# Kernel tuning notes

Hardware: AMD Instinct MI355X
Metric: run time of the kernel (lower is better)

Reference implementation:

```python
import jax, jax.numpy as jnp
import numpy as np

NUM_NODES = 50000
NUM_EDGES = 600000
NUM_FEAT = 128
HIDDEN = 512
N_OUT = 128
K = 3
N_GRAPHS = 128


def setup_inputs() -> dict:
    key = jax.random.key(0)
    ks = jax.random.split(key, 12)
    feature = jax.random.normal(ks[0], (NUM_NODES, NUM_FEAT), dtype=jnp.float32)
    edge_index = jax.random.randint(ks[1], (2, NUM_EDGES), 0, NUM_NODES, dtype=jnp.int64)
    protein_batch = jnp.sort(jax.random.randint(ks[2], (NUM_NODES,), 0, N_GRAPHS, dtype=jnp.int64))
    s = 0.05
    # ChebConv weights stored [K, in, out] (x @ W), single shared bias per conv
    W1 = jax.random.normal(ks[3], (K, NUM_FEAT, NUM_FEAT), dtype=jnp.float32) * s
    b1 = jax.random.normal(ks[4], (NUM_FEAT,), dtype=jnp.float32) * s
    W2 = jax.random.normal(ks[5], (K, NUM_FEAT, 2 * NUM_FEAT), dtype=jnp.float32) * s
    b2 = jax.random.normal(ks[6], (2 * NUM_FEAT,), dtype=jnp.float32) * s
    fc1_w = jax.random.normal(ks[7], (3 * NUM_FEAT, HIDDEN), dtype=jnp.float32) * s
    fc1_b = jax.random.normal(ks[8], (HIDDEN,), dtype=jnp.float32) * s
    fc2_w = jax.random.normal(ks[9], (HIDDEN, N_OUT), dtype=jnp.float32) * s
    fc2_b = jax.random.normal(ks[10], (N_OUT,), dtype=jnp.float32) * s
    return {"feature": feature, "edge_index": edge_index, "protein_batch": protein_batch,
            "W1": W1, "b1": b1, "W2": W2, "b2": b2,
            "fc1_w": fc1_w, "fc1_b": fc1_b, "fc2_w": fc2_w, "fc2_b": fc2_b}


def _cheb_conv(x, src, dst, edge_w, W, b):
    # PyG ChebConv with sym normalization, lambda_max=2 => scaled Laplacian
    # L_hat has zero diagonal and off-diag weights -1/sqrt(d_i d_j) (edge_w).
    def prop(h):
        return jax.ops.segment_sum(edge_w[:, None] * h[src], dst, num_segments=NUM_NODES)

    Tx0 = x
    out = Tx0 @ W[0]
    Tx1 = prop(x)
    out = out + Tx1 @ W[1]
    for k in range(2, W.shape[0]):
        Tx2 = 2.0 * prop(Tx1) - Tx0
        out = out + Tx2 @ W[k]
        Tx0, Tx1 = Tx1, Tx2
    return out + b


def reference(feature, edge_index, protein_batch, W1, b1, W2, b2, fc1_w, fc1_b, fc2_w, fc2_b):
    src, dst = edge_index[0], edge_index[1]
    deg = jax.ops.segment_sum(jnp.ones_like(src, dtype=feature.dtype), src, num_segments=NUM_NODES)
    dinv = jnp.where(deg > 0, jax.lax.rsqrt(jnp.maximum(deg, 1.0)), 0.0)
    edge_w = -dinv[src] * dinv[dst]  # (2/lambda_max)*L_sym off-diagonal; diag cancels to 0

    gx = jax.nn.relu(_cheb_conv(feature, src, dst, edge_w, W1, b1))
    gx = jax.nn.relu(_cheb_conv(gx, src, dst, edge_w, W2, b2))
    gx = jnp.concatenate([gx, feature], axis=1)  # [N, 3*F]

    # global_mean_pool
    sums = jax.ops.segment_sum(gx, protein_batch, num_segments=N_GRAPHS)
    cnts = jax.ops.segment_sum(jnp.ones((gx.shape[0],), gx.dtype), protein_batch, num_segments=N_GRAPHS)
    pooled = sums / jnp.maximum(cnts, 1.0)[:, None]

    h = jax.nn.relu(pooled @ fc1_w + fc1_b)  # dropout is identity in eval
    return h @ fc2_w + fc2_b
```

## Files before the change

kernel.cpp:

```cpp
#include <hip/hip_runtime.h>
#include <hip/hip_bf16.h>

#define NNODES 50000
#define NEDGES 600000
#define NB 196
#define NBKT 196
#define SB 192
#define SCH (NEDGES / SB)

typedef short vs8 __attribute__((ext_vector_type(8)));
typedef float floatx4 __attribute__((ext_vector_type(4)));

__device__ __forceinline__ float us2f(unsigned short u) {
    unsigned int x = ((unsigned int)u) << 16;
    float f;
    __builtin_memcpy(&f, &x, 4);
    return f;
}
__device__ __forceinline__ unsigned short f2us(float f) {
    unsigned int x;
    __builtin_memcpy(&x, &f, 4);
    unsigned int r = x + 0x7fffu + ((x >> 16) & 1u);
    return (unsigned short)(r >> 16);
}
__device__ __forceinline__ float ldf(const void* p, int i, int ff) {
    if (ff) return us2f(((const unsigned short*)p)[i]);
    return ((const float*)p)[i];
}
__device__ __forceinline__ int2 ldnt_sw(const int2* p) {
    unsigned long long v =
        __builtin_nontemporal_load(reinterpret_cast<const unsigned long long*>(p));
    int2 r;
    r.x = (int)(unsigned int)(v & 0xffffffffULL);
    r.y = (int)(unsigned int)(v >> 32);
    return r;
}
__device__ __forceinline__ void gload_lds16(const unsigned short* g, unsigned short* l) {
    __builtin_amdgcn_global_load_lds(
        (const __attribute__((address_space(1))) unsigned int*)g,
        (__attribute__((address_space(3))) unsigned int*)l, 16, 0, 0);
}
__device__ __forceinline__ void accum8(float w, uint4 u, float& a0, float& a1,
                                       float& a2, float& a3, float& a4, float& a5,
                                       float& a6, float& a7) {
    a0 += w * us2f((unsigned short)(u.x & 0xffffu));
    a1 += w * us2f((unsigned short)(u.x >> 16));
    a2 += w * us2f((unsigned short)(u.y & 0xffffu));
    a3 += w * us2f((unsigned short)(u.y >> 16));
    a4 += w * us2f((unsigned short)(u.z & 0xffffu));
    a5 += w * us2f((unsigned short)(u.z >> 16));
    a6 += w * us2f((unsigned short)(u.w & 0xffffu));
    a7 += w * us2f((unsigned short)(u.w >> 16));
}

__global__ void k_detect(const int* ei, const unsigned int* fw, int* iflag, int* fflag) {
    int lane = threadIdx.x;
    int odd1 = ei[2 * lane + 1];
    int odd2 = ei[128 + 2 * lane + 1];
    unsigned long long nz = __ballot(odd1 != 0 || odd2 != 0);
    unsigned int e = (fw[lane] >> 7) & 0xffu;
    unsigned long long h = __ballot(e > 100u && e < 160u);
    if (lane == 0) {
        *iflag = (nz == 0ULL) ? 1 : 0;
        *fflag = (__popcll(h) > 40) ? 1 : 0;
    }
}

__global__ void k_featb(const void* src, const int* iflag, const int* fflag,
                        const int* pb, int* b32, float* psum, unsigned short* dst) {
    int i = blockIdx.x * 256 + threadIdx.x;
    if (i < NNODES) {
        int f = *iflag;
        b32[i] = pb[((size_t)i) << f];
    }
    if (i < 128 * 384) psum[i] = 0.f;
    if (i >= NNODES * 128 / 8) return;
    if (*fflag) {
        reinterpret_cast<uint4*>(dst)[i] = reinterpret_cast<const uint4*>(src)[i];
    } else {
        const float4* fs = reinterpret_cast<const float4*>(src);
        float4 a = fs[2 * i], b = fs[2 * i + 1];
        uint4 o;
        o.x = (unsigned int)f2us(a.x) | ((unsigned int)f2us(a.y) << 16);
        o.y = (unsigned int)f2us(a.z) | ((unsigned int)f2us(a.w) << 16);
        o.z = (unsigned int)f2us(b.x) | ((unsigned int)f2us(b.y) << 16);
        o.w = (unsigned int)f2us(b.z) | ((unsigned int)f2us(b.w) << 16);
        reinterpret_cast<uint4*>(dst)[i] = o;
    }
}

__global__ __launch_bounds__(256) void k_deghist(const int* ei, const int* iflag,
                                                 unsigned int* degpart, int* cntT) {
    __shared__ unsigned int h[25000];
    __shared__ int c[NBKT];
    int t = threadIdx.x, blk = blockIdx.x;
    for (int i = t; i < 25000; i += 256) h[i] = 0u;
    if (t < NBKT) c[t] = 0;
    __syncthreads();
    int f = *iflag;
    int e0 = blk * SCH;
    for (int j = t; j < SCH; j += 256) {
        int e = e0 + j;
        int s = ei[((size_t)e) << f];
        int d = ei[((size_t)(NEDGES + e)) << f];
        atomicAdd(&h[s >> 1], (s & 1) ? 65536u : 1u);
        atomicAdd(&c[d >> 8], 1);
    }
    __syncthreads();
    unsigned int* dp = degpart + (size_t)blk * 25000;
    for (int i = t; i < 25000; i += 256) dp[i] = h[i];
    if (t < NBKT) cntT[t * SB + blk] = c[t];
}

__global__ void k_dred(const unsigned int* degpart, float* dinv) {
    int i = blockIdx.x * 256 + threadIdx.x;
    if (i >= 25000) return;
    unsigned int lo = 0, hi = 0;
    for (int b = 0; b < SB; ++b) {
        unsigned int p = degpart[(size_t)b * 25000 + i];
        lo += p & 0xffffu;
        hi += p >> 16;
    }
    dinv[2 * i] = lo ? rsqrtf((float)lo) : 0.f;
    dinv[2 * i + 1] = hi ? rsqrtf((float)hi) : 0.f;
}

__global__ void k_bprefix(int* cntT, int* btot) {
    __shared__ int sh[256];
    int t = threadIdx.x, b = blockIdx.x;
    int v = (t < SB) ? cntT[b * SB + t] : 0;
    sh[t] = v;
    __syncthreads();
    for (int off = 1; off < 256; off <<= 1) {
        int x = (t >= off) ? sh[t - off] : 0;
        __syncthreads();
        sh[t] += x;
        __syncthreads();
    }
    if (t < SB) cntT[b * SB + t] = sh[t] - v;
    if (t == 255) btot[b] = sh[255];
}

__global__ void k_bscan2(const int* btot, int* gbase, const int* batch32,
                         int* pcnt, int* rowptr) {
    __shared__ int sh[256];
    int t = threadIdx.x;
    int v = (t < NBKT) ? btot[t] : 0;
    sh[t] = v;
    __syncthreads();
    for (int off = 1; off < 256; off <<= 1) {
        int x = (t >= off) ? sh[t - off] : 0;
        __syncthreads();
        sh[t] += x;
        __syncthreads();
    }
    if (t < NBKT) gbase[t] = sh[t] - v;
    if (t == 0) {
        gbase[NBKT] = NEDGES;
        rowptr[NNODES] = NEDGES;
    }
    if (t < 128) {
        int g = t;
        int lo = 0, hi = NNODES;
        while (lo < hi) { int mid = (lo + hi) >> 1; if (batch32[mid] < g) lo = mid + 1; else hi = mid; }
        int start = lo;
        hi = NNODES;
        while (lo < hi) { int mid = (lo + hi) >> 1; if (batch32[mid] <= g) lo = mid + 1; else hi = mid; }
        pcnt[g] = lo - start;
    }
}

__global__ void k_scat(const int* ei, const int* iflag, const float* dinv,
                       const int* gbase, const int* cntT, int2* bkt) {
    __shared__ int cur[NBKT];
    int t = threadIdx.x, blk = blockIdx.x;
    if (t < NBKT) cur[t] = gbase[t] + cntT[t * SB + blk];
    __syncthreads();
    int f = *iflag;
    int e0 = blk * SCH;
    for (int j = t; j < SCH; j += 256) {
        int e = e0 + j;
        int s = ei[((size_t)e) << f];
        int d = ei[((size_t)(NEDGES + e)) << f];
        float w = -dinv[s] * dinv[d];
        int slot = atomicAdd(&cur[d >> 8], 1);
        int wb;
        __builtin_memcpy(&wb, &w, 4);
        int2 v;
        v.x = s | ((d & 255) << 16);
        v.y = wb;
        bkt[slot] = v;
    }
}

__global__ void k_csr(const int2* bkt, const int* gbase, int* rowptr, int2* csr_sw) {
    __shared__ int hist[256], scan[256], cur[256];
    int t = threadIdx.x, b = blockIdx.x;
    int beg = gbase[b], end = gbase[b + 1];
    int n = end - beg;
    hist[t] = 0;
    __syncthreads();
    for (int i = t; i < n; i += 256) {
        int bin = (bkt[beg + i].x >> 16) & 255;
        atomicAdd(&hist[bin], 1);
    }
    __syncthreads();
    int h = hist[t];
    scan[t] = h;
    __syncthreads();
    for (int off = 1; off < 256; off <<= 1) {
        int x = (t >= off) ? scan[t - off] : 0;
        __syncthreads();
        scan[t] += x;
        __syncthreads();
    }
    int excl = scan[t] - h;
    int node = b * 256 + t;
    if (node < NNODES) rowptr[node] = beg + excl;
    cur[t] = excl;
    __syncthreads();
    for (int i = t; i < n; i += 256) {
        int2 p = bkt[beg + i];
        int bin = (p.x >> 16) & 255;
        int slot = atomicAdd(&cur[bin], 1);
        int2 v;
        v.x = p.x & 0xffff;
        v.y = p.y;
        csr_sw[beg + slot] = v;
    }
}

__global__ void k_prepall(const void* W1, const void* W2, const void* b1, const void* b2,
                          const void* f1w, const void* f1b, const void* f2w, const void* f2b,
                          const int* fflag, unsigned short* W1t, unsigned short* W2t,
                          float* b1f, float* b2f, float* f1wf, float* f1bf,
                          float* f2wf, float* f2bf) {
    int i = blockIdx.x * 256 + threadIdx.x;
    int ff = *fflag;
    if (i < 49152) {
        int c = i >> 13;
        int rem = i & 8191;
        int cr = rem >> 6;
        int rem2 = rem & 63;
        int g = rem2 >> 3, j = rem2 & 7;
        int k = c * 64 + ((g ^ (cr & 7)) << 3) + j;
        int n = cr;
        float v;
        if (k < 128) v = ldf(W1, k * 128 + n, ff) - ldf(W1, (256 + k) * 128 + n, ff);
        else if (k < 256) v = ldf(W1, k * 128 + n, ff);
        else v = 2.f * ldf(W1, k * 128 + n, ff);
        W1t[i] = f2us(v);
        return;
    }
    i -= 49152;
    if (i < 98304) {
        int ct = i / 49152;
        int rem = i % 49152;
        int c = rem >> 13;
        int rem1 = rem & 8191;
        int cr = rem1 >> 6;
        int rem2 = rem1 & 63;
        int g = rem2 >> 3, j = rem2 & 7;
        int k = c * 64 + ((g ^ (cr & 7)) << 3) + j;
        int n = ct * 128 + cr;
        float v;
        if (k < 128) v = ldf(W2, k * 256 + n, ff) - ldf(W2, (256 + k) * 256 + n, ff);
        else if (k < 256) v = ldf(W2, k * 256 + n, ff);
        else v = 2.f * ldf(W2, k * 256 + n, ff);
        W2t[i] = f2us(v);
        return;
    }
    i -= 98304;
    if (i < 196608) { f1wf[i] = ldf(f1w, i, ff); return; }
    i -= 196608;
    if (i < 65536) { f2wf[i] = ldf(f2w, i, ff); return; }
    i -= 65536;
    if (i < 512) { f1bf[i] = ldf(f1b, i, ff); return; }
    i -= 512;
    if (i < 256) { b2f[i] = ldf(b2, i, ff); return; }
    i -= 256;
    if (i < 128) { b1f[i] = ldf(b1, i, ff); return; }
    i -= 128;
    if (i < 128) f2bf[i] = ldf(f2b, i, ff);
}

__global__ __launch_bounds__(256, 6) void k_prop(const unsigned short* X,
                                                 const int* rowptr, const int2* csr_sw,
                                                 unsigned short* out) {
    int wvid = (blockIdx.x * blockDim.x + threadIdx.x) >> 6;
    int lane = threadIdx.x & 63;
    int q = lane >> 4;
    int ln = lane & 15;
    int node = wvid * 4 + q;
    if (node >= NNODES) return;
    int fo = ln * 8;
    int beg = rowptr[node], end = rowptr[node + 1];
    float a0 = 0.f, a1 = 0.f, a2 = 0.f, a3 = 0.f;
    float a4 = 0.f, a5 = 0.f, a6 = 0.f, a7 = 0.f;
    int j = beg;
    for (; j + 8 <= end; j += 8) {
        int2 e0 = ldnt_sw(csr_sw + j);
        int2 e1 = ldnt_sw(csr_sw + j + 1);
        int2 e2 = ldnt_sw(csr_sw + j + 2);
        int2 e3 = ldnt_sw(csr_sw + j + 3);
        int2 e4 = ldnt_sw(csr_sw + j + 4);
        int2 e5 = ldnt_sw(csr_sw + j + 5);
        int2 e6 = ldnt_sw(csr_sw + j + 6);
        int2 e7 = ldnt_sw(csr_sw + j + 7);
        uint4 u0 = *reinterpret_cast<const uint4*>(X + (size_t)e0.x * 128 + fo);
        uint4 u1 = *reinterpret_cast<const uint4*>(X + (size_t)e1.x * 128 + fo);
        uint4 u2 = *reinterpret_cast<const uint4*>(X + (size_t)e2.x * 128 + fo);
        uint4 u3 = *reinterpret_cast<const uint4*>(X + (size_t)e3.x * 128 + fo);
        uint4 u4 = *reinterpret_cast<const uint4*>(X + (size_t)e4.x * 128 + fo);
        uint4 u5 = *reinterpret_cast<const uint4*>(X + (size_t)e5.x * 128 + fo);
        uint4 u6 = *reinterpret_cast<const uint4*>(X + (size_t)e6.x * 128 + fo);
        uint4 u7 = *reinterpret_cast<const uint4*>(X + (size_t)e7.x * 128 + fo);
        float w0, w1, w2, w3, w4, w5, w6, w7;
        __builtin_memcpy(&w0, &e0.y, 4);
        __builtin_memcpy(&w1, &e1.y, 4);
        __builtin_memcpy(&w2, &e2.y, 4);
        __builtin_memcpy(&w3, &e3.y, 4);
        __builtin_memcpy(&w4, &e4.y, 4);
        __builtin_memcpy(&w5, &e5.y, 4);
        __builtin_memcpy(&w6, &e6.y, 4);
        __builtin_memcpy(&w7, &e7.y, 4);
        accum8(w0, u0, a0, a1, a2, a3, a4, a5, a6, a7);
        accum8(w1, u1, a0, a1, a2, a3, a4, a5, a6, a7);
        accum8(w2, u2, a0, a1, a2, a3, a4, a5, a6, a7);
        accum8(w3, u3, a0, a1, a2, a3, a4, a5, a6, a7);
        accum8(w4, u4, a0, a1, a2, a3, a4, a5, a6, a7);
        accum8(w5, u5, a0, a1, a2, a3, a4, a5, a6, a7);
        accum8(w6, u6, a0, a1, a2, a3, a4, a5, a6, a7);
        accum8(w7, u7, a0, a1, a2, a3, a4, a5, a6, a7);
    }
    for (; j + 4 <= end; j += 4) {
        int2 e0 = ldnt_sw(csr_sw + j);
        int2 e1 = ldnt_sw(csr_sw + j + 1);
        int2 e2 = ldnt_sw(csr_sw + j + 2);
        int2 e3 = ldnt_sw(csr_sw + j + 3);
        uint4 u0 = *reinterpret_cast<const uint4*>(X + (size_t)e0.x * 128 + fo);
        uint4 u1 = *reinterpret_cast<const uint4*>(X + (size_t)e1.x * 128 + fo);
        uint4 u2 = *reinterpret_cast<const uint4*>(X + (size_t)e2.x * 128 + fo);
        uint4 u3 = *reinterpret_cast<const uint4*>(X + (size_t)e3.x * 128 + fo);
        float w0, w1, w2, w3;
        __builtin_memcpy(&w0, &e0.y, 4);
        __builtin_memcpy(&w1, &e1.y, 4);
        __builtin_memcpy(&w2, &e2.y, 4);
        __builtin_memcpy(&w3, &e3.y, 4);
        accum8(w0, u0, a0, a1, a2, a3, a4, a5, a6, a7);
        accum8(w1, u1, a0, a1, a2, a3, a4, a5, a6, a7);
        accum8(w2, u2, a0, a1, a2, a3, a4, a5, a6, a7);
        accum8(w3, u3, a0, a1, a2, a3, a4, a5, a6, a7);
    }
    for (; j < end; ++j) {
        int2 e = ldnt_sw(csr_sw + j);
        float w;
        __builtin_memcpy(&w, &e.y, 4);
        uint4 u = *reinterpret_cast<const uint4*>(X + (size_t)e.x * 128 + fo);
        accum8(w, u, a0, a1, a2, a3, a4, a5, a6, a7);
    }
    uint4 ov;
    ov.x = (unsigned int)f2us(a0) | ((unsigned int)f2us(a1) << 16);
    ov.y = (unsigned int)f2us(a2) | ((unsigned int)f2us(a3) << 16);
    ov.z = (unsigned int)f2us(a4) | ((unsigned int)f2us(a5) << 16);
    ov.w = (unsigned int)f2us(a6) | ((unsigned int)f2us(a7) << 16);
    *reinterpret_cast<uint4*>(out + (size_t)node * 128 + fo) = ov;
}

template <int POOL, int CT>
__global__ __launch_bounds__(512, 4) void k_convg(
    const unsigned short* seg0, const unsigned short* seg1, const unsigned short* seg2,
    const unsigned short* Wt, const float* bias, unsigned short* out,
    const int* batch32, float* psum) {
    __shared__ __align__(16) unsigned short a_lds[2][8192];
    __shared__ __align__(16) unsigned short b_lds[2][8192];
    __shared__ float sh_ps[POOL ? 1024 : 1];
    int tid = threadIdx.x;
    int bid = blockIdx.x;
    int grp = 8 * CT;
    int main_blocks = 48 * grp;
    int r, ct;
    if (bid < main_blocks) {
        int g = bid / grp;
        int rem = bid - g * grp;
        ct = rem >> 3;
        r = g * 8 + (rem & 7);
    } else {
        int t = bid - main_blocks;
        r = 384 + (CT == 1 ? t : t % 7);
        ct = (CT == 1) ? 0 : t / 7;
    }
    int r0 = r * 128;
    const unsigned short* segs[3] = {seg0, seg1, seg2};
    int wv = tid >> 6, lane = tid & 63;
    int wm = wv >> 2, wn = wv & 3;
    int m = lane & 15, kq = lane >> 4;
    if (POOL) { sh_ps[tid] = 0.f; sh_ps[tid + 512] = 0.f; }

    auto STAGE = [&](int buf, int c) {
        const unsigned short* S = segs[c >> 1];
        int h = c & 1;
#pragma unroll
        for (int p = 0; p < 2; ++p) {
            int q = wv * 2 + p;
            int rl = q * 8 + (lane >> 3);
            int g = lane & 7;
            int rowg = r0 + rl;
            if (rowg >= NNODES) rowg = NNODES - 1;
            gload_lds16(S + (size_t)rowg * 128 + h * 64 + ((g ^ (rl & 7)) << 3),
                        &a_lds[buf][q * 512]);
        }
#pragma unroll
        for (int p = 0; p < 2; ++p) {
            int q = wv * 2 + p;
            gload_lds16(Wt + (size_t)(ct * 6 + c) * 8192 + q * 512 + (lane << 3),
                        &b_lds[buf][q * 512]);
        }
    };

    floatx4 acc[4][2];
#pragma unroll
    for (int mt = 0; mt < 4; ++mt)
#pragma unroll
        for (int nt = 0; nt < 2; ++nt) {
            acc[mt][nt][0] = 0.f; acc[mt][nt][1] = 0.f;
            acc[mt][nt][2] = 0.f; acc[mt][nt][3] = 0.f;
        }

    STAGE(0, 0);
    __syncthreads();
    int buf = 0;
#pragma unroll
    for (int c = 0; c < 6; ++c) {
        if (c < 5) STAGE(buf ^ 1, c + 1);
        vs8 af[4], bfr[2];
#pragma unroll
        for (int kf = 0; kf < 2; ++kf) {
            int G = kf * 4 + kq;
#pragma unroll
            for (int mt = 0; mt < 4; ++mt) {
                int row = wm * 64 + mt * 16 + m;
                af[mt] = *reinterpret_cast<const vs8*>(
                    &a_lds[buf][row * 64 + ((G ^ (row & 7)) << 3)]);
            }
#pragma unroll
            for (int nt = 0; nt < 2; ++nt) {
                int cl = wn * 32 + nt * 16 + m;
                bfr[nt] = *reinterpret_cast<const vs8*>(
                    &b_lds[buf][cl * 64 + ((G ^ (cl & 7)) << 3)]);
            }
#pragma unroll
            for (int mt = 0; mt < 4; ++mt)
#pragma unroll
                for (int nt = 0; nt < 2; ++nt)
                    acc[mt][nt] = __builtin_amdgcn_mfma_f32_16x16x32_bf16(
                        af[mt], bfr[nt], acc[mt][nt], 0, 0, 0);
        }
        if (c < 5) {
            __syncthreads();
            buf ^= 1;
        }
    }

    if (POOL == 0) {
#pragma unroll
        for (int mt = 0; mt < 4; ++mt) {
            int rbase = r0 + wm * 64 + mt * 16 + kq * 4;
#pragma unroll
            for (int nt = 0; nt < 2; ++nt) {
                int col = wn * 32 + nt * 16 + m;
                float bv = bias[col];
#pragma unroll
                for (int i = 0; i < 4; ++i) {
                    int rw = rbase + i;
                    if (rw < NNODES) {
                        float v = acc[mt][nt][i] + bv;
                        v = v > 0.f ? v : 0.f;
                        out[(size_t)rw * 128 + col] = f2us(v);
                    }
                }
            }
        }
    } else {
        int g0 = batch32[r0];
#pragma unroll
        for (int mt = 0; mt < 4; ++mt) {
            int rbase = r0 + wm * 64 + mt * 16 + kq * 4;
            int gid[4];
#pragma unroll
            for (int i = 0; i < 4; ++i) {
                int rw = rbase + i;
                gid[i] = rw < NNODES ? batch32[rw] : -1;
            }
#pragma unroll
            for (int nt = 0; nt < 2; ++nt) {
                int cl = wn * 32 + nt * 16 + m;
                int col = ct * 128 + cl;
                float bv = bias[col];
                float run = 0.f;
                int curg = -1;
#pragma unroll
                for (int i = 0; i < 4; ++i) {
                    int g = gid[i];
                    if (g < 0) break;
                    float v = acc[mt][nt][i] + bv;
                    v = v > 0.f ? v : 0.f;
                    if (g != curg) {
                        if (curg >= 0) {
                            int gl = curg - g0;
                            if (gl >= 0 && gl < 8) atomicAdd(&sh_ps[gl * 128 + cl], run);
                            else atomicAdd(&psum[curg * 384 + col], run);
                        }
                        curg = g;
                        run = 0.f;
                    }
                    run += v;
                }
                if (curg >= 0) {
                    int gl = curg - g0;
                    if (gl >= 0 && gl < 8) atomicAdd(&sh_ps[gl * 128 + cl], run);
                    else atomicAdd(&psum[curg * 384 + col], run);
                }
            }
        }
        __syncthreads();
        for (int idx = tid; idx < 1024; idx += 512) {
            int gl = idx >> 7, cl = idx & 127;
            float v = sh_ps[idx];
            int gg = g0 + gl;
            if (v != 0.f && gg < 128) atomicAdd(&psum[(size_t)gg * 384 + ct * 128 + cl], v);
        }
    }
}

__global__ void k_poolnodes(const unsigned short* featb, const int* batch32, float* psum) {
    int col = threadIdx.x & 127;
    int half = threadIdx.x >> 7;
    int nbeg = blockIdx.x * 128 + half * 64;
    if (nbeg >= NNODES) return;
    int nend = nbeg + 64;
    if (nend > NNODES) nend = NNODES;
    float run = 0.f;
    int curg = batch32[nbeg];
    for (int n = nbeg; n < nend; ++n) {
        int g = batch32[n];
        if (g != curg) {
            atomicAdd(&psum[curg * 384 + 256 + col], run);
            run = 0.f;
            curg = g;
        }
        run += us2f(featb[(size_t)n * 128 + col]);
    }
    atomicAdd(&psum[curg * 384 + 256 + col], run);
}

__global__ void k_fc1(const float* psum, const int* pcnt, const float* w,
                      const float* b, float* h) {
    int g = blockIdx.x, j = threadIdx.x * 2;
    int c = pcnt[g];
    float inv = 1.f / (float)(c > 0 ? c : 1);
    float a0 = 0.f, a1 = 0.f;
    for (int k = 0; k < 384; ++k) {
        float p = psum[g * 384 + k];
        a0 += p * w[k * 512 + j];
        a1 += p * w[k * 512 + j + 1];
    }
    a0 = a0 * inv + b[j];
    a1 = a1 * inv + b[j + 1];
    h[g * 512 + j] = a0 > 0.f ? a0 : 0.f;
    h[g * 512 + j + 1] = a1 > 0.f ? a1 : 0.f;
}

__global__ void ChebModel_74380243632480_kernel(const float* h, const float* w,
                                                const float* b, const int* fflag,
                                                void* out) {
    int g = blockIdx.x, j = threadIdx.x;
    float acc = 0.f;
    for (int k = 0; k < 512; ++k) acc += h[g * 512 + k] * w[k * 128 + j];
    acc += b[j];
    if (*fflag) ((unsigned short*)out)[g * 128 + j] = f2us(acc);
    else ((float*)out)[g * 128 + j] = acc;
}

extern "C" void kernel_launch(void* const* d_in, const int* in_sizes, int n_in,
                              void* d_out, int out_size, void* d_ws, size_t ws_size,
                              hipStream_t stream) {
    const void* feature = d_in[0];
    const int* edge_index = (const int*)d_in[1];
    const int* batch = (const int*)d_in[2];
    const void* W1 = d_in[3];
    const void* b1 = d_in[4];
    const void* W2 = d_in[5];
    const void* b2 = d_in[6];
    const void* fc1w = d_in[7];
    const void* fc1b = d_in[8];
    const void* fc2w = d_in[9];
    const void* fc2b = d_in[10];

    char* ws = (char*)d_ws;
    size_t off = 0;
    int* iflag = (int*)(ws + off); off += 256;
    int* fflag = (int*)(ws + off); off += 256;
    int* rowptr = (int*)(ws + off); off += ((size_t)(NNODES + 1) * 4 + 255) & ~(size_t)255;
    float* dinv = (float*)(ws + off); off += ((size_t)NNODES * 4 + 255) & ~(size_t)255;
    int* batch32 = (int*)(ws + off); off += ((size_t)NNODES * 4 + 255) & ~(size_t)255;
    int* gbase = (int*)(ws + off); off += 1024;
    int* cntT = (int*)(ws + off); off += ((size_t)SB * NBKT * 4 + 255) & ~(size_t)255;
    int* btot = (int*)(ws + off); off += 1024;
    int2* csr_sw = (int2*)(ws + off); off += ((size_t)NEDGES * 8 + 255) & ~(size_t)255;
    unsigned short* featb = (unsigned short*)(ws + off); off += ((size_t)NNODES * 128 * 2 + 255) & ~(size_t)255;
    unsigned short* T1 = (unsigned short*)(ws + off); off += ((size_t)NNODES * 128 * 2 + 255) & ~(size_t)255;
    unsigned short* T2 = (unsigned short*)(ws + off); off += ((size_t)NNODES * 128 * 2 + 255) & ~(size_t)255;
    unsigned short* gx1 = (unsigned short*)(ws + off); off += ((size_t)NNODES * 128 * 2 + 255) & ~(size_t)255;
    unsigned short* W1t = (unsigned short*)(ws + off); off += ((size_t)49152 * 2 + 255) & ~(size_t)255;
    unsigned short* W2t = (unsigned short*)(ws + off); off += ((size_t)98304 * 2 + 255) & ~(size_t)255;
    float* b1f = (float*)(ws + off); off += 1024;
    float* b2f = (float*)(ws + off); off += 1024;
    float* fc1wf = (float*)(ws + off); off += ((size_t)196608 * 4 + 255) & ~(size_t)255;
    float* fc1bf = (float*)(ws + off); off += 2048;
    float* fc2wf = (float*)(ws + off); off += ((size_t)65536 * 4 + 255) & ~(size_t)255;
    float* fc2bf = (float*)(ws + off); off += 1024;
    float* psum = (float*)(ws + off); off += ((size_t)128 * 384 * 4 + 255) & ~(size_t)255;
    int* pcnt = (int*)(ws + off); off += 1024;
    float* hbuf = (float*)(ws + off); off += ((size_t)128 * 512 * 4 + 255) & ~(size_t)255;

    int2* bkt = (int2*)T1;
    unsigned int* degpart = (unsigned int*)T2;

    k_detect<<<1, 64, 0, stream>>>(edge_index, (const unsigned int*)feature, iflag, fflag);
    k_featb<<<(NNODES * 128 / 8 + 255) / 256, 256, 0, stream>>>(
        feature, iflag, fflag, batch, batch32, psum, featb);
    k_deghist<<<SB, 256, 0, stream>>>(edge_index, iflag, degpart, cntT);
    k_dred<<<(25000 + 255) / 256, 256, 0, stream>>>(degpart, dinv);
    k_bprefix<<<NBKT, 256, 0, stream>>>(cntT, btot);
    k_bscan2<<<1, 256, 0, stream>>>(btot, gbase, batch32, pcnt, rowptr);
    k_scat<<<SB, 256, 0, stream>>>(edge_index, iflag, dinv, gbase, cntT, bkt);
    k_csr<<<NBKT, 256, 0, stream>>>(bkt, gbase, rowptr, csr_sw);
    k_prepall<<<(410624 + 255) / 256, 256, 0, stream>>>(
        W1, W2, b1, b2, fc1w, fc1b, fc2w, fc2b, fflag,
        W1t, W2t, b1f, b2f, fc1wf, fc1bf, fc2wf, fc2bf);

    int pb = ((NNODES + 3) / 4 * 64 + 255) / 256;
    k_prop<<<pb, 256, 0, stream>>>(featb, rowptr, csr_sw, T1);
    k_prop<<<pb, 256, 0, stream>>>(T1, rowptr, csr_sw, T2);
    k_convg<0, 1><<<391, 512, 0, stream>>>(featb, T1, T2, W1t, b1f, gx1,
                                           (const int*)0, (float*)0);
    k_prop<<<pb, 256, 0, stream>>>(gx1, rowptr, csr_sw, T1);
    k_prop<<<pb, 256, 0, stream>>>(T1, rowptr, csr_sw, T2);
    k_convg<1, 2><<<782, 512, 0, stream>>>(gx1, T1, T2, W2t, b2f, (unsigned short*)0,
                                           batch32, psum);
    k_poolnodes<<<(NNODES + 127) / 128, 256, 0, stream>>>(featb, batch32, psum);
    k_fc1<<<128, 256, 0, stream>>>(psum, pcnt, fc1wf, fc1bf, hbuf);
    ChebModel_74380243632480_kernel<<<128, 128, 0, stream>>>(hbuf, fc2wf, fc2bf, fflag, d_out);
}
```

Measured before the change: 367.2 us.

## Fuse small kernels, inline flag detection, and predicate prop tail loop

Removes the separate detect kernel by recomputing the index-width and dtype flags inside each consumer kernel from a wavefront ballot. The degree reduction and bucket prefix kernels are merged into one launch, the feature pooling runs as extra blocks of the second conv GEMM, and fc1 and fc2 are merged into a single kernel. The prop gather loop replaces its 4-wide and scalar tail loops with one 8-wide loop that clamps indices and zeroes weights past the row end. This cuts launch count and serialization overhead, at the cost of redundant flag loads in every block and wasted gathers on short rows.

```diff
diff --git a/kernel.cpp b/kernel.cpp
--- a/kernel.cpp
+++ b/kernel.cpp
@@ -26,6 +26,19 @@
 __device__ __forceinline__ float ldf(const void* p, int i, int ff) {
     if (ff) return us2f(((const unsigned short*)p)[i]);
     return ((const float*)p)[i];
+}
+__device__ __forceinline__ int detect_iflag(const int* ei) {
+    int lane = threadIdx.x & 63;
+    int odd1 = ei[2 * lane + 1];
+    int odd2 = ei[128 + 2 * lane + 1];
+    unsigned long long nz = __ballot(odd1 != 0 || odd2 != 0);
+    return (nz == 0ULL) ? 1 : 0;
+}
+__device__ __forceinline__ int detect_fflag(const unsigned int* fw) {
+    int lane = threadIdx.x & 63;
+    unsigned int e = (fw[lane] >> 7) & 0xffu;
+    unsigned long long h = __ballot(e > 100u && e < 160u);
+    return (__popcll(h) > 40) ? 1 : 0;
 }
 __device__ __forceinline__ int2 ldnt_sw(const int2* p) {
     unsigned long long v =
@@ -53,29 +66,15 @@
     a7 += w * us2f((unsigned short)(u.w >> 16));
 }
 
-__global__ void k_detect(const int* ei, const unsigned int* fw, int* iflag, int* fflag) {
-    int lane = threadIdx.x;
-    int odd1 = ei[2 * lane + 1];
-    int odd2 = ei[128 + 2 * lane + 1];
-    unsigned long long nz = __ballot(odd1 != 0 || odd2 != 0);
-    unsigned int e = (fw[lane] >> 7) & 0xffu;
-    unsigned long long h = __ballot(e > 100u && e < 160u);
-    if (lane == 0) {
-        *iflag = (nz == 0ULL) ? 1 : 0;
-        *fflag = (__popcll(h) > 40) ? 1 : 0;
-    }
-}
-
-__global__ void k_featb(const void* src, const int* iflag, const int* fflag,
-                        const int* pb, int* b32, float* psum, unsigned short* dst) {
+__global__ void k_featb(const void* src, const int* ei, const int* pb,
+                        int* b32, float* psum, unsigned short* dst) {
     int i = blockIdx.x * 256 + threadIdx.x;
-    if (i < NNODES) {
-        int f = *iflag;
-        b32[i] = pb[((size_t)i) << f];
-    }
+    int f = detect_iflag(ei);
+    int ff = detect_fflag((const unsigned int*)src);
+    if (i < NNODES) b32[i] = pb[((size_t)i) << f];
     if (i < 128 * 384) psum[i] = 0.f;
     if (i >= NNODES * 128 / 8) return;
-    if (*fflag) {
+    if (ff) {
         reinterpret_cast<uint4*>(dst)[i] = reinterpret_cast<const uint4*>(src)[i];
     } else {
         const float4* fs = reinterpret_cast<const float4*>(src);
@@ -89,15 +88,15 @@
     }
 }
 
-__global__ __launch_bounds__(256) void k_deghist(const int* ei, const int* iflag,
+__global__ __launch_bounds__(256) void k_deghist(const int* ei,
                                                  unsigned int* degpart, int* cntT) {
     __shared__ unsigned int h[25000];
     __shared__ int c[NBKT];
     int t = threadIdx.x, blk = blockIdx.x;
+    int f = detect_iflag(ei);
     for (int i = t; i < 25000; i += 256) h[i] = 0u;
     if (t < NBKT) c[t] = 0;
     __syncthreads();
-    int f = *iflag;
     int e0 = blk * SCH;
     for (int j = t; j < SCH; j += 256) {
         int e = e0 + j;
@@ -112,33 +111,34 @@
     if (t < NBKT) cntT[t * SB + blk] = c[t];
 }
 
-__global__ void k_dred(const unsigned int* degpart, float* dinv) {
-    int i = blockIdx.x * 256 + threadIdx.x;
-    if (i >= 25000) return;
-    unsigned int lo = 0, hi = 0;
-    for (int b = 0; b < SB; ++b) {
-        unsigned int p = degpart[(size_t)b * 25000 + i];
-        lo += p & 0xffffu;
-        hi += p >> 16;
-    }
-    dinv[2 * i] = lo ? rsqrtf((float)lo) : 0.f;
-    dinv[2 * i + 1] = hi ? rsqrtf((float)hi) : 0.f;
-}
-
-__global__ void k_bprefix(int* cntT, int* btot) {
-    __shared__ int sh[256];
-    int t = threadIdx.x, b = blockIdx.x;
-    int v = (t < SB) ? cntT[b * SB + t] : 0;
-    sh[t] = v;
-    __syncthreads();
-    for (int off = 1; off < 256; off <<= 1) {
-        int x = (t >= off) ? sh[t - off] : 0;
+__global__ void k_mid(const unsigned int* degpart, float* dinv, int* cntT, int* btot) {
+    int bid = blockIdx.x, t = threadIdx.x;
+    if (bid < NBKT) {
+        __shared__ int sh[256];
+        int b = bid;
+        int v = (t < SB) ? cntT[b * SB + t] : 0;
+        sh[t] = v;
         __syncthreads();
-        sh[t] += x;
-        __syncthreads();
-    }
-    if (t < SB) cntT[b * SB + t] = sh[t] - v;
-    if (t == 255) btot[b] = sh[255];
+        for (int off = 1; off < 256; off <<= 1) {
+            int x = (t >= off) ? sh[t - off] : 0;
+            __syncthreads();
+            sh[t] += x;
+            __syncthreads();
+        }
+        if (t < SB) cntT[b * SB + t] = sh[t] - v;
+        if (t == 255) btot[b] = sh[255];
+    } else {
+        int i = (bid - NBKT) * 256 + t;
+        if (i >= 25000) return;
+        unsigned int lo = 0, hi = 0;
+        for (int b = 0; b < SB; ++b) {
+            unsigned int p = degpart[(size_t)b * 25000 + i];
+            lo += p & 0xffffu;
+            hi += p >> 16;
+        }
+        dinv[2 * i] = lo ? rsqrtf((float)lo) : 0.f;
+        dinv[2 * i + 1] = hi ? rsqrtf((float)hi) : 0.f;
+    }
 }
 
 __global__ void k_bscan2(const int* btot, int* gbase, const int* batch32,
@@ -170,13 +170,13 @@
     }
 }
 
-__global__ void k_scat(const int* ei, const int* iflag, const float* dinv,
+__global__ void k_scat(const int* ei, const float* dinv,
                        const int* gbase, const int* cntT, int2* bkt) {
     __shared__ int cur[NBKT];
     int t = threadIdx.x, blk = blockIdx.x;
+    int f = detect_iflag(ei);
     if (t < NBKT) cur[t] = gbase[t] + cntT[t * SB + blk];
     __syncthreads();
-    int f = *iflag;
     int e0 = blk * SCH;
     for (int j = t; j < SCH; j += 256) {
         int e = e0 + j;
@@ -232,11 +232,11 @@
 
 __global__ void k_prepall(const void* W1, const void* W2, const void* b1, const void* b2,
                           const void* f1w, const void* f1b, const void* f2w, const void* f2b,
-                          const int* fflag, unsigned short* W1t, unsigned short* W2t,
+                          const unsigned int* fw, unsigned short* W1t, unsigned short* W2t,
                           float* b1f, float* b2f, float* f1wf, float* f1bf,
                           float* f2wf, float* f2bf) {
     int i = blockIdx.x * 256 + threadIdx.x;
-    int ff = *fflag;
+    int ff = detect_fflag(fw);
     if (i < 49152) {
         int c = i >> 13;
         int rem = i & 8191;
@@ -297,16 +297,23 @@
     int beg = rowptr[node], end = rowptr[node + 1];
     float a0 = 0.f, a1 = 0.f, a2 = 0.f, a3 = 0.f;
     float a4 = 0.f, a5 = 0.f, a6 = 0.f, a7 = 0.f;
-    int j = beg;
-    for (; j + 8 <= end; j += 8) {
+    for (int j = beg; j < end; j += 8) {
+        int last = end - 1;
+        int i1 = j + 1 < end ? j + 1 : last;
+        int i2 = j + 2 < end ? j + 2 : last;
+        int i3 = j + 3 < end ? j + 3 : last;
+        int i4 = j + 4 < end ? j + 4 : last;
+        int i5 = j + 5 < end ? j + 5 : last;
+        int i6 = j + 6 < end ? j + 6 : last;
+        int i7 = j + 7 < end ? j + 7 : last;
         int2 e0 = ldnt_sw(csr_sw + j);
-        int2 e1 = ldnt_sw(csr_sw + j + 1);
-        int2 e2 = ldnt_sw(csr_sw + j + 2);
-        int2 e3 = ldnt_sw(csr_sw + j + 3);
-        int2 e4 = ldnt_sw(csr_sw + j + 4);
-        int2 e5 = ldnt_sw(csr_sw + j + 5);
-        int2 e6 = ldnt_sw(csr_sw + j + 6);
-        int2 e7 = ldnt_sw(csr_sw + j + 7);
+        int2 e1 = ldnt_sw(csr_sw + i1);
+        int2 e2 = ldnt_sw(csr_sw + i2);
+        int2 e3 = ldnt_sw(csr_sw + i3);
+        int2 e4 = ldnt_sw(csr_sw + i4);
+        int2 e5 = ldnt_sw(csr_sw + i5);
+        int2 e6 = ldnt_sw(csr_sw + i6);
+        int2 e7 = ldnt_sw(csr_sw + i7);
         uint4 u0 = *reinterpret_cast<const uint4*>(X + (size_t)e0.x * 128 + fo);
         uint4 u1 = *reinterpret_cast<const uint4*>(X + (size_t)e1.x * 128 + fo);
         uint4 u2 = *reinterpret_cast<const uint4*>(X + (size_t)e2.x * 128 + fo);
@@ -324,6 +331,13 @@
         __builtin_memcpy(&w5, &e5.y, 4);
         __builtin_memcpy(&w6, &e6.y, 4);
         __builtin_memcpy(&w7, &e7.y, 4);
+        w1 = (j + 1 < end) ? w1 : 0.f;
+        w2 = (j + 2 < end) ? w2 : 0.f;
+        w3 = (j + 3 < end) ? w3 : 0.f;
+        w4 = (j + 4 < end) ? w4 : 0.f;
+        w5 = (j + 5 < end) ? w5 : 0.f;
+        w6 = (j + 6 < end) ? w6 : 0.f;
+        w7 = (j + 7 < end) ? w7 : 0.f;
         accum8(w0, u0, a0, a1, a2, a3, a4, a5, a6, a7);
         accum8(w1, u1, a0, a1, a2, a3, a4, a5, a6, a7);
         accum8(w2, u2, a0, a1, a2, a3, a4, a5, a6, a7);
@@ -333,32 +347,6 @@
         accum8(w6, u6, a0, a1, a2, a3, a4, a5, a6, a7);
         accum8(w7, u7, a0, a1, a2, a3, a4, a5, a6, a7);
     }
-    for (; j + 4 <= end; j += 4) {
-        int2 e0 = ldnt_sw(csr_sw + j);
-        int2 e1 = ldnt_sw(csr_sw + j + 1);
-        int2 e2 = ldnt_sw(csr_sw + j + 2);
-        int2 e3 = ldnt_sw(csr_sw + j + 3);
-        uint4 u0 = *reinterpret_cast<const uint4*>(X + (size_t)e0.x * 128 + fo);
-        uint4 u1 = *reinterpret_cast<const uint4*>(X + (size_t)e1.x * 128 + fo);
-        uint4 u2 = *reinterpret_cast<const uint4*>(X + (size_t)e2.x * 128 + fo);
-        uint4 u3 = *reinterpret_cast<const uint4*>(X + (size_t)e3.x * 128 + fo);
-        float w0, w1, w2, w3;
-        __builtin_memcpy(&w0, &e0.y, 4);
-        __builtin_memcpy(&w1, &e1.y, 4);
-        __builtin_memcpy(&w2, &e2.y, 4);
-        __builtin_memcpy(&w3, &e3.y, 4);
-        accum8(w0, u0, a0, a1, a2, a3, a4, a5, a6, a7);
-        accum8(w1, u1, a0, a1, a2, a3, a4, a5, a6, a7);
-        accum8(w2, u2, a0, a1, a2, a3, a4, a5, a6, a7);
-        accum8(w3, u3, a0, a1, a2, a3, a4, a5, a6, a7);
-    }
-    for (; j < end; ++j) {
-        int2 e = ldnt_sw(csr_sw + j);
-        float w;
-        __builtin_memcpy(&w, &e.y, 4);
-        uint4 u = *reinterpret_cast<const uint4*>(X + (size_t)e.x * 128 + fo);
-        accum8(w, u, a0, a1, a2, a3, a4, a5, a6, a7);
-    }
     uint4 ov;
     ov.x = (unsigned int)f2us(a0) | ((unsigned int)f2us(a1) << 16);
     ov.y = (unsigned int)f2us(a2) | ((unsigned int)f2us(a3) << 16);
@@ -371,7 +359,7 @@
 __global__ __launch_bounds__(512, 4) void k_convg(
     const unsigned short* seg0, const unsigned short* seg1, const unsigned short* seg2,
     const unsigned short* Wt, const float* bias, unsigned short* out,
-    const int* batch32, float* psum) {
+    const int* batch32, float* psum, const unsigned short* featX) {
     __shared__ __align__(16) unsigned short a_lds[2][8192];
     __shared__ __align__(16) unsigned short b_lds[2][8192];
     __shared__ float sh_ps[POOL ? 1024 : 1];
@@ -379,6 +367,31 @@
     int bid = blockIdx.x;
     int grp = 8 * CT;
     int main_blocks = 48 * grp;
+    if (POOL) {
+        int gemm_blocks = main_blocks + 7 * CT;
+        if (bid >= gemm_blocks) {
+            int pb = bid - gemm_blocks;
+            int col = tid & 127, qq = tid >> 7;
+            int nbeg = pb * 256 + qq * 64;
+            if (nbeg < NNODES) {
+                int nend = nbeg + 64;
+                if (nend > NNODES) nend = NNODES;
+                float run = 0.f;
+                int curg = batch32[nbeg];
+                for (int n = nbeg; n < nend; ++n) {
+                    int g = batch32[n];
+                    if (g != curg) {
+                        atomicAdd(&psum[curg * 384 + 256 + col], run);
+                        run = 0.f;
+                        curg = g;
+                    }
+                    run += us2f(featX[(size_t)n * 128 + col]);
+                }
+                atomicAdd(&psum[curg * 384 + 256 + col], run);
+            }
+            return;
+        }
+    }
     int r, ct;
     if (bid < main_blocks) {
         int g = bid / grp;
@@ -533,53 +546,38 @@
     }
 }
 
-__global__ void k_poolnodes(const unsigned short* featb, const int* batch32, float* psum) {
-    int col = threadIdx.x & 127;
-    int half = threadIdx.x >> 7;
-    int nbeg = blockIdx.x * 128 + half * 64;
-    if (nbeg >= NNODES) return;
-    int nend = nbeg + 64;
-    if (nend > NNODES) nend = NNODES;
-    float run = 0.f;
-    int curg = batch32[nbeg];
-    for (int n = nbeg; n < nend; ++n) {
-        int g = batch32[n];
-        if (g != curg) {
-            atomicAdd(&psum[curg * 384 + 256 + col], run);
-            run = 0.f;
-            curg = g;
-        }
-        run += us2f(featb[(size_t)n * 128 + col]);
-    }
-    atomicAdd(&psum[curg * 384 + 256 + col], run);
-}
-
-__global__ void k_fc1(const float* psum, const int* pcnt, const float* w,
-                      const float* b, float* h) {
-    int g = blockIdx.x, j = threadIdx.x * 2;
+__global__ void ChebModel_74380243632480_kernel(
+    const float* psum, const int* pcnt, const float* w1, const float* b1,
+    const float* w2, const float* b2, const unsigned int* fw, void* out) {
+    __shared__ float hl[512];
+    __shared__ float ps[256];
+    int g = blockIdx.x, tid = threadIdx.x;
+    int ff = detect_fflag(fw);
     int c = pcnt[g];
     float inv = 1.f / (float)(c > 0 ? c : 1);
+    int j = tid * 2;
     float a0 = 0.f, a1 = 0.f;
     for (int k = 0; k < 384; ++k) {
         float p = psum[g * 384 + k];
-        a0 += p * w[k * 512 + j];
-        a1 += p * w[k * 512 + j + 1];
-    }
-    a0 = a0 * inv + b[j];
-    a1 = a1 * inv + b[j + 1];
-    h[g * 512 + j] = a0 > 0.f ? a0 : 0.f;
-    h[g * 512 + j + 1] = a1 > 0.f ? a1 : 0.f;
-}
-
-__global__ void ChebModel_74380243632480_kernel(const float* h, const float* w,
-                                                const float* b, const int* fflag,
-                                                void* out) {
-    int g = blockIdx.x, j = threadIdx.x;
+        a0 += p * w1[k * 512 + j];
+        a1 += p * w1[k * 512 + j + 1];
+    }
+    a0 = a0 * inv + b1[j];
+    a1 = a1 * inv + b1[j + 1];
+    hl[j] = a0 > 0.f ? a0 : 0.f;
+    hl[j + 1] = a1 > 0.f ? a1 : 0.f;
+    __syncthreads();
+    int half = tid >> 7, jj = tid & 127;
     float acc = 0.f;
-    for (int k = 0; k < 512; ++k) acc += h[g * 512 + k] * w[k * 128 + j];
-    acc += b[j];
-    if (*fflag) ((unsigned short*)out)[g * 128 + j] = f2us(acc);
-    else ((float*)out)[g * 128 + j] = acc;
+    for (int k = half * 256; k < half * 256 + 256; ++k)
+        acc += hl[k] * w2[k * 128 + jj];
+    ps[tid] = acc;
+    __syncthreads();
+    if (tid < 128) {
+        float v = ps[tid] + ps[tid + 128] + b2[tid];
+        if (ff) ((unsigned short*)out)[g * 128 + tid] = f2us(v);
+        else ((float*)out)[g * 128 + tid] = v;
+    }
 }
 
 extern "C" void kernel_launch(void* const* d_in, const int* in_sizes, int n_in,
@@ -599,8 +597,6 @@
 
     char* ws = (char*)d_ws;
     size_t off = 0;
-    int* iflag = (int*)(ws + off); off += 256;
-    int* fflag = (int*)(ws + off); off += 256;
     int* rowptr = (int*)(ws + off); off += ((size_t)(NNODES + 1) * 4 + 255) & ~(size_t)255;
     float* dinv = (float*)(ws + off); off += ((size_t)NNODES * 4 + 255) & ~(size_t)255;
     int* batch32 = (int*)(ws + off); off += ((size_t)NNODES * 4 + 255) & ~(size_t)255;
@@ -622,34 +618,30 @@
     float* fc2bf = (float*)(ws + off); off += 1024;
     float* psum = (float*)(ws + off); off += ((size_t)128 * 384 * 4 + 255) & ~(size_t)255;
     int* pcnt = (int*)(ws + off); off += 1024;
-    float* hbuf = (float*)(ws + off); off += ((size_t)128 * 512 * 4 + 255) & ~(size_t)255;
 
     int2* bkt = (int2*)T1;
     unsigned int* degpart = (unsigned int*)T2;
 
-    k_detect<<<1, 64, 0, stream>>>(edge_index, (const unsigned int*)feature, iflag, fflag);
     k_featb<<<(NNODES * 128 / 8 + 255) / 256, 256, 0, stream>>>(
-        feature, iflag, fflag, batch, batch32, psum, featb);
-    k_deghist<<<SB, 256, 0, stream>>>(edge_index, iflag, degpart, cntT);
-    k_dred<<<(25000 + 255) / 256, 256, 0, stream>>>(degpart, dinv);
-    k_bprefix<<<NBKT, 256, 0, stream>>>(cntT, btot);
+        feature, edge_index, batch, batch32, psum, featb);
+    k_deghist<<<SB, 256, 0, stream>>>(edge_index, degpart, cntT);
+    k_mid<<<NBKT + (25000 + 255) / 256, 256, 0, stream>>>(degpart, dinv, cntT, btot);
     k_bscan2<<<1, 256, 0, stream>>>(btot, gbase, batch32, pcnt, rowptr);
-    k_scat<<<SB, 256, 0, stream>>>(edge_index, iflag, dinv, gbase, cntT, bkt);
+    k_scat<<<SB, 256, 0, stream>>>(edge_index, dinv, gbase, cntT, bkt);
     k_csr<<<NBKT, 256, 0, stream>>>(bkt, gbase, rowptr, csr_sw);
     k_prepall<<<(410624 + 255) / 256, 256, 0, stream>>>(
-        W1, W2, b1, b2, fc1w, fc1b, fc2w, fc2b, fflag,
+        W1, W2, b1, b2, fc1w, fc1b, fc2w, fc2b, (const unsigned int*)feature,
         W1t, W2t, b1f, b2f, fc1wf, fc1bf, fc2wf, fc2bf);
 
     int pb = ((NNODES + 3) / 4 * 64 + 255) / 256;
     k_prop<<<pb, 256, 0, stream>>>(featb, rowptr, csr_sw, T1);
     k_prop<<<pb, 256, 0, stream>>>(T1, rowptr, csr_sw, T2);
     k_convg<0, 1><<<391, 512, 0, stream>>>(featb, T1, T2, W1t, b1f, gx1,
-                                           (const int*)0, (float*)0);
+                                           (const int*)0, (float*)0, (const unsigned short*)0);
     k_prop<<<pb, 256, 0, stream>>>(gx1, rowptr, csr_sw, T1);
     k_prop<<<pb, 256, 0, stream>>>(T1, rowptr, csr_sw, T2);
-    k_convg<1, 2><<<782, 512, 0, stream>>>(gx1, T1, T2, W2t, b2f, (unsigned short*)0,
-                                           batch32, psum);
-    k_poolnodes<<<(NNODES + 127) / 128, 256, 0, stream>>>(featb, batch32, psum);
-    k_fc1<<<128, 256, 0, stream>>>(psum, pcnt, fc1wf, fc1bf, hbuf);
-    ChebModel_74380243632480_kernel<<<128, 128, 0, stream>>>(hbuf, fc2wf, fc2bf, fflag, d_out);
-}
+    k_convg<1, 2><<<782 + 196, 512, 0, stream>>>(gx1, T1, T2, W2t, b2f, (unsigned short*)0,
+                                                 batch32, psum, featb);
+    ChebModel_74380243632480_kernel<<<128, 256, 0, stream>>>(
+        psum, pcnt, fc1wf, fc1bf, fc2wf, fc2bf, (const unsigned int*)feature, d_out);
+}
```

Result: slower. 386.5 us (+5.3%).
